# Kernel tuning notes

Measured on AMD Instinct MI355X. Metric: run time of the kernel, lower is better.

The kernel has to match this reference:

```python
import jax, jax.numpy as jnp
import numpy as np

H = 16          # n_heads
DH = 128        # head_dim
DR = 64         # rope_dim
DC = DH - DR    # content_dim = 64
THETA = 10000.0
SCALE = 1.0 / np.sqrt(DH)


def _rope_tables(T, dtype):
    inv = 1.0 / (THETA ** (jnp.arange(0, DR, 2, dtype=jnp.float32) / DR))  # [DR/2]
    t = jnp.arange(T, dtype=jnp.float32)
    freqs = jnp.outer(t, inv)  # [T, DR/2]
    return jnp.cos(freqs).astype(dtype), jnp.sin(freqs).astype(dtype)


def _apply_rope(x, cos, sin):
    # x: [B,H,T,DR]; cos/sin: [T,DR/2] broadcast over B,H
    d = x.shape[-1] // 2
    x1, x2 = x[..., :d], x[..., d:]
    return jnp.concatenate([x1 * cos - x2 * sin, x1 * sin + x2 * cos], axis=-1)


def setup_inputs() -> dict:
    key = jax.random.key(0)
    ks = jax.random.split(key, 9)
    B, T, D = 1, 2048, 2048
    s = 0.02
    return {
        "x": jax.random.normal(ks[0], (B, T, D), jnp.float32),
        "Wq_down": jax.random.normal(ks[1], (D, 512), jnp.float32) * s,
        "Wq_up": jax.random.normal(ks[2], (512, H * DC), jnp.float32) * s,
        "Wq_rope": jax.random.normal(ks[3], (D, H * DR), jnp.float32) * s,
        "Wkv_down": jax.random.normal(ks[4], (D, 512), jnp.float32) * s,
        "Wk_up": jax.random.normal(ks[5], (512, H * DC), jnp.float32) * s,
        "Wv_up": jax.random.normal(ks[6], (512, H * DH), jnp.float32) * s,
        "Wk_rope": jax.random.normal(ks[7], (D, H * DR), jnp.float32) * s,
        "Wo": jax.random.normal(ks[8], (H * DH, D), jnp.float32) * s,
    }


def reference(x, Wq_down, Wq_up, Wq_rope, Wkv_down, Wk_up, Wv_up, Wk_rope, Wo):
    B, T, D = x.shape
    # low-rank query path: down then up, content part only
    q_content = ((x @ Wq_down) @ Wq_up).reshape(B, T, H, DC).transpose(0, 2, 1, 3)
    q_pos = (x @ Wq_rope).reshape(B, T, H, DR).transpose(0, 2, 1, 3)
    kv_latent = x @ Wkv_down                    # [B,T,d_latent]
    k_pos = (x @ Wk_rope).reshape(B, T, H, DR).transpose(0, 2, 1, 3)

    cos, sin = _rope_tables(T, x.dtype)
    q_pos = _apply_rope(q_pos, cos, sin)
    k_pos = _apply_rope(k_pos, cos, sin)

    k_content = (kv_latent @ Wk_up).reshape(B, T, H, DC).transpose(0, 2, 1, 3)
    v = (kv_latent @ Wv_up).reshape(B, T, H, DH).transpose(0, 2, 1, 3)

    q = jnp.concatenate([q_content, q_pos], axis=-1)  # [B,H,T,DH]
    k = jnp.concatenate([k_content, k_pos], axis=-1)  # [B,H,T,DH]

    scores = jnp.einsum("bhtd,bhsd->bhts", q, k) * SCALE
    causal = jnp.tril(jnp.ones((T, T), dtype=bool))
    scores = jnp.where(causal, scores, jnp.finfo(scores.dtype).min)
    attn = jax.nn.softmax(scores, axis=-1)
    out = jnp.einsum("bhts,bhsd->bhtd", attn, v)       # [B,H,T,DH]
    out = out.transpose(0, 2, 1, 3).reshape(B, T, H * DH)
    return out @ Wo
```

## Files before the change

### kernel.cpp

```cpp
#include <hip/hip_runtime.h>
#include <math.h>

#define T_SEQ 2048
#define D_MODEL 2048
#define H_HEADS 16
#define DH 128
#define DR 64
#define DC 64
#define D_LAT 512
#define SEGLEN 14
#define NSEG_TOT 46
#define QSCALE (0.08838834764831845f * 1.4426950408889634f)

typedef __attribute__((ext_vector_type(8))) short short8;
typedef __attribute__((ext_vector_type(4))) short short4v;
typedef __attribute__((ext_vector_type(4))) float f32x4;

#if __has_builtin(__builtin_amdgcn_exp2f)
#define EXP2(x) __builtin_amdgcn_exp2f(x)
#else
#define EXP2(x) exp2f(x)
#endif

__device__ __forceinline__ float bf2f(short b) {
    unsigned u = ((unsigned)(unsigned short)b) << 16;
    return __builtin_bit_cast(float, u);
}
__device__ __forceinline__ short f2bf(float f) {
    unsigned u = __builtin_bit_cast(unsigned, f);
    unsigned r = u + 0x7fffu + ((u >> 16) & 1u);
    return (short)(r >> 16);
}
__device__ __forceinline__ short f2bf_trunc(float f) {
    return (short)(__builtin_bit_cast(unsigned, f) >> 16);
}

#define GLD_LDS(gp, lp) \
    __builtin_amdgcn_global_load_lds( \
        (const __attribute__((address_space(1))) void*)(gp), \
        (__attribute__((address_space(3))) void*)(lp), 16, 0, 0)

__device__ __forceinline__ void ct_tile(float (*tile)[33],
                                        const float* __restrict__ W,
                                        short* __restrict__ Wt,
                                        int R, int C, int ldo, int rel) {
    int bx = rel % (C / 32), by = rel / (C / 32);
    int c0 = bx * 32, r0 = by * 32;
    int tx = threadIdx.x & 31, ty = threadIdx.x >> 5;
    #pragma unroll
    for (int i = 0; i < 4; ++i)
        tile[ty + i * 8][tx] = W[(size_t)(r0 + ty + i * 8) * C + c0 + tx];
    __syncthreads();
    #pragma unroll
    for (int i = 0; i < 4; ++i)
        Wt[(size_t)(c0 + ty + i * 8) * ldo + r0 + tx] = f2bf(tile[tx][ty + i * 8]);
    __syncthreads();
}

__global__ __launch_bounds__(256) void prep(const float* __restrict__ x,
                                            short* __restrict__ xb,
                                            const float* __restrict__ Wqd,
                                            const float* __restrict__ Wkvd,
                                            const float* __restrict__ Wqr,
                                            const float* __restrict__ Wkr,
                                            const float* __restrict__ Wqu,
                                            const float* __restrict__ Wku,
                                            const float* __restrict__ Wvu,
                                            const float* __restrict__ Wo,
                                            short* __restrict__ WdT,
                                            short* __restrict__ WupT2,
                                            short* __restrict__ WoT) {
    __shared__ float tile[32][33];
    int bid = blockIdx.x;
    if (bid < 4096) {
        int i = bid * 1024 + threadIdx.x * 4;
        float4 f = *(const float4*)&x[i];
        short4v o;
        o.x = f2bf(f.x); o.y = f2bf(f.y); o.z = f2bf(f.z); o.w = f2bf(f.w);
        *(short4v*)&xb[i] = o;
    } else if (bid < 5120) {
        ct_tile(tile, Wqd,  WdT + (size_t)0 * 2048,    2048, 512,  2048, bid - 4096);
    } else if (bid < 6144) {
        ct_tile(tile, Wkvd, WdT + (size_t)512 * 2048,  2048, 512,  2048, bid - 5120);
    } else if (bid < 8192) {
        ct_tile(tile, Wqr,  WdT + (size_t)1024 * 2048, 2048, 1024, 2048, bid - 6144);
    } else if (bid < 10240) {
        ct_tile(tile, Wkr,  WdT + (size_t)2048 * 2048, 2048, 1024, 2048, bid - 8192);
    } else if (bid < 10752) {
        ct_tile(tile, Wqu,  WupT2 + (size_t)0 * 512,    512, 1024, 512, bid - 10240);
    } else if (bid < 11264) {
        ct_tile(tile, Wku,  WupT2 + (size_t)1024 * 512, 512, 1024, 512, bid - 10752);
    } else if (bid < 12288) {
        ct_tile(tile, Wvu,  WupT2 + (size_t)2048 * 512, 512, 2048, 512, bid - 11264);
    } else {
        ct_tile(tile, Wo,   WoT, 2048, 2048, 2048, bid - 12288);
    }
}

__global__ __launch_bounds__(256) void transpose_bf16(const short* __restrict__ in,
                                                      short* __restrict__ outb,
                                                      int ldi) {
    __shared__ short tile[64][65];
    int c0 = blockIdx.x * 64, t0 = blockIdx.y * 64;
    int tx = threadIdx.x & 31, ty = threadIdx.x >> 5;
    #pragma unroll
    for (int i = 0; i < 8; ++i) {
        int r = ty + i * 8;
        int vv = *(const int*)&in[(size_t)(t0 + r) * ldi + c0 + tx * 2];
        tile[r][tx * 2]     = (short)(vv & 0xffff);
        tile[r][tx * 2 + 1] = (short)(((unsigned)vv) >> 16);
    }
    __syncthreads();
    #pragma unroll
    for (int i = 0; i < 8; ++i) {
        int c = ty + i * 8;
        unsigned lo = (unsigned short)tile[tx * 2][c];
        unsigned hi = (unsigned short)tile[tx * 2 + 1][c];
        *(int*)&outb[(size_t)(c0 + c) * 2048 + t0 + tx * 2] = (int)(lo | (hi << 16));
    }
}

__global__ __launch_bounds__(256) void gemm_bt(const short* __restrict__ A,
                                               const short* __restrict__ A2,
                                               const short* __restrict__ Bt,
                                               short* __restrict__ C0,
                                               short* __restrict__ C1,
                                               short* __restrict__ C2,
                                               short* __restrict__ C3,
                                               int N, int Kblk,
                                               int lda, int ldb, int ldc,
                                               int ncut, int scut, float cscale) {
    __shared__ short As[128 * 32];
    __shared__ short Bs[128 * 32];
    const int tid = threadIdx.x;
    const int wave = tid >> 6, lane = tid & 63;
    const int lin = blockIdx.x;
    const int X = N >> 7, Xq = X >> 2;
    const int xcd = lin & 7;
    int r = lin >> 3;
    const int bx = (xcd & 3) * Xq + (r % Xq); r /= Xq;
    const int by = (xcd >> 2) * 8 + (r & 7);
    const int bz = r >> 3;
    const int row0 = by * 128, col0 = bx * 128;
    const int kbase = bz * Kblk;
    const short* Ause = (col0 < ncut) ? A : A2;
    short* Cuse = (bz == 0) ? C0 : (bz == 1) ? C1 : (bz == 2) ? C2 : C3;
    const int wr = (wave >> 1) * 64, wc = (wave & 1) * 64;
    const int lr = lane & 15, quad = lane >> 4;

    f32x4 acc[4][4];
    #pragma unroll
    for (int i = 0; i < 4; ++i)
        #pragma unroll
        for (int j = 0; j < 4; ++j) acc[i][j] = (f32x4){0.f, 0.f, 0.f, 0.f};

    for (int k0 = kbase; k0 < kbase + Kblk; k0 += 32) {
        __syncthreads();
        #pragma unroll
        for (int it = 0; it < 2; ++it) {
            int idx = wave * 64 + it * 256 + lane;
            const short* ga = Ause + (size_t)(row0 + (idx >> 2)) * lda + k0 + (idx & 3) * 8;
            const short* gb = Bt   + (size_t)(col0 + (idx >> 2)) * ldb + k0 + (idx & 3) * 8;
            int lds0 = (wave * 64 + it * 256) * 8;
            GLD_LDS(ga, &As[lds0]);
            GLD_LDS(gb, &Bs[lds0]);
        }
        __syncthreads();

        short8 af[4], bfr[4];
        #pragma unroll
        for (int i = 0; i < 4; ++i)
            af[i] = *(const short8*)&As[(wr + i * 16 + lr) * 32 + quad * 8];
        #pragma unroll
        for (int j = 0; j < 4; ++j)
            bfr[j] = *(const short8*)&Bs[(wc + j * 16 + lr) * 32 + quad * 8];
        #pragma unroll
        for (int i = 0; i < 4; ++i)
            #pragma unroll
            for (int j = 0; j < 4; ++j)
                acc[i][j] = __builtin_amdgcn_mfma_f32_16x16x32_bf16(af[i], bfr[j],
                                                                   acc[i][j], 0, 0, 0);
    }

    const float sc = (col0 < scut) ? cscale : 1.0f;
    #pragma unroll
    for (int i = 0; i < 4; ++i) {
        int rb = row0 + wr + i * 16 + quad * 4;
        #pragma unroll
        for (int j = 0; j < 4; ++j) {
            int c = col0 + wc + j * 16 + lr;
            #pragma unroll
            for (int rr = 0; rr < 4; ++rr)
                Cuse[(size_t)(rb + rr) * ldc + c] = f2bf(acc[i][j][rr] * sc);
        }
    }
}

__global__ __launch_bounds__(192) void finish_down(short* __restrict__ cat,
                                                   const short* __restrict__ pdown) {
    const int t = blockIdx.x;
    const int k8 = threadIdx.x * 8;
    const int c0 = ((k8 >> 5) << 6) + (k8 & 31);
    const size_t lo = (size_t)t * 3072 + c0;
    const size_t hi = lo + 32;
    short8 al = *(const short8*)&cat[lo];
    short8 ah = *(const short8*)&cat[hi];
    short8 bl = *(const short8*)&pdown[lo];
    short8 bh = *(const short8*)&pdown[hi];
    float xl[8], xh[8];
    #pragma unroll
    for (int j = 0; j < 8; ++j) {
        xl[j] = bf2f(al[j]) + bf2f(bl[j]);
        xh[j] = bf2f(ah[j]) + bf2f(bh[j]);
    }
    if (c0 >= 1024) {
        float sc = (c0 < 2048) ? QSCALE : 1.0f;
        #pragma unroll
        for (int j = 0; j < 8; ++j) {
            int i = (c0 & 31) + j;
            float freq = (float)t * __powf(10000.0f, -(float)i / 32.0f);
            float cs = __cosf(freq), sn = __sinf(freq);
            float r1 = (xl[j] * cs - xh[j] * sn) * sc;
            float r2 = (xl[j] * sn + xh[j] * cs) * sc;
            xl[j] = r1; xh[j] = r2;
        }
    }
    short8 ol, oh;
    #pragma unroll
    for (int j = 0; j < 8; ++j) { ol[j] = f2bf(xl[j]); oh[j] = f2bf(xh[j]); }
    *(short8*)&cat[lo] = ol;
    *(short8*)&cat[hi] = oh;
}

__global__ __launch_bounds__(256) void add_out_f32(const short* __restrict__ p0,
                                                   const short* __restrict__ p1,
                                                   float* __restrict__ out) {
    int i = (blockIdx.x * 256 + threadIdx.x) * 4;
    short4v a = *(const short4v*)&p0[i];
    short4v b = *(const short4v*)&p1[i];
    float4 o;
    o.x = bf2f(a.x) + bf2f(b.x);
    o.y = bf2f(a.y) + bf2f(b.y);
    o.z = bf2f(a.z) + bf2f(b.z);
    o.w = bf2f(a.w) + bf2f(b.w);
    *(float4*)&out[i] = o;
}

__global__ __launch_bounds__(256) void attn_mla_split(const short* __restrict__ qkup,
                                                      const short* __restrict__ cat,
                                                      const short* __restrict__ vT,
                                                      short* __restrict__ slabA,
                                                      short* __restrict__ slabB,
                                                      float* __restrict__ lpart) {
    const int lin = blockIdx.x;
    const int xcd = lin & 7;
    int k_ = lin >> 3;
    const int h = xcd + 8 * (k_ & 1);
    const int pp = k_ >> 1;
    int qt = 0, s = 0, acc = 0;
    #pragma unroll
    for (int q = 0; q < 16; ++q) {
        const int ns = (4 * q + 4 + SEGLEN - 1) / SEGLEN;
        if (pp >= acc) { qt = q; s = pp - acc; }
        acc += ns;
    }
    const int nchunk = 4 * qt + 4;
    const int nsq = (nchunk + SEGLEN - 1) / SEGLEN;
    const int cbase = nchunk / nsq, crem = nchunk % nsq;
    const int c0 = s * cbase + (s < crem ? s : crem);
    const int c1 = c0 + cbase + (s < crem ? 1 : 0);

    const int tid = threadIdx.x;
    const int wave = tid >> 6, lane = tid & 63;
    const int lr = lane & 15, quad = lane >> 4;

    __shared__ short Ks[2][32 * 128];
    __shared__ short Vst[2][128 * 32];
    __shared__ short Ps[4][2][16 * 40];

    const short8 ones = {0x3F80, 0x3F80, 0x3F80, 0x3F80,
                         0x3F80, 0x3F80, 0x3F80, 0x3F80};

    const int Q0 = qt * 128;
    const int qrowA = Q0 + wave * 16;
    const int qrowB = qrowA + 64;

    short8 qf[2][4];
    #pragma unroll
    for (int sb = 0; sb < 2; ++sb) {
        int t = (sb ? qrowB : qrowA) + lr;
        #pragma unroll
        for (int kci = 0; kci < 4; ++kci) {
            const short* src = (kci < 2)
                ? qkup + (size_t)t * 4096 + h * 64
                : cat + (size_t)t * 3072 + 1024 + h * 64;
            qf[sb][kci] = *(const short8*)&src[(kci & 1) * 32 + quad * 8];
        }
    }

    const int idx = wave * 64 + lane;
    const int key = idx >> 4;
    const int cg = (idx & 15) ^ (key & 15);
    const short* kp0 = (cg < 8)
        ? qkup + (size_t)key * 4096 + 1024 + h * 64 + cg * 8
        : cat + (size_t)key * 3072 + 2048 + h * 64 + (cg - 8) * 8;
    const int kst = (cg < 8) ? 4096 : 3072;
    const short* kp1 = kp0 + (size_t)16 * kst;
    const int dd = idx >> 2;
    const int scg = (idx & 3) ^ (dd & 3);
    const short* vp0 = vT + (size_t)(h * 128 + dd) * 2048 + scg * 8;
    const short* vp1 = vp0 + (size_t)64 * 2048;
    kp0 += (size_t)c0 * 32 * kst; kp1 += (size_t)c0 * 32 * kst;
    vp0 += c0 * 32;               vp1 += c0 * 32;
    const int kadv = 32 * kst;
    const int vadv = 32;
    const int ldsA = (wave * 64) * 8;
    const int ldsB = (wave * 64 + 256) * 8;

    f32x4 Oacc[2][8];
    #pragma unroll
    for (int sb = 0; sb < 2; ++sb)
        #pragma unroll
        for (int d = 0; d < 8; ++d) Oacc[sb][d] = (f32x4){0.f, 0.f, 0.f, 0.f};
    f32x4 Lacc[2];
    Lacc[0] = (f32x4){0.f, 0.f, 0.f, 0.f};
    Lacc[1] = (f32x4){0.f, 0.f, 0.f, 0.f};

    GLD_LDS(kp0, &Ks[0][ldsA]);
    GLD_LDS(kp1, &Ks[0][ldsB]);
    GLD_LDS(vp0, &Vst[0][ldsA]);
    GLD_LDS(vp1, &Vst[0][ldsB]);
    kp0 += kadv; kp1 += kadv; vp0 += vadv; vp1 += vadv;

    int cur = 0;
    for (int c = c0; c < c1; ++c) {
        const int s0 = c * 32;
        const bool havenext = (c + 1 < c1);
        if (havenext) {
            GLD_LDS(kp0, &Ks[cur ^ 1][ldsA]);
            GLD_LDS(kp1, &Ks[cur ^ 1][ldsB]);
            GLD_LDS(vp0, &Vst[cur ^ 1][ldsA]);
            GLD_LDS(vp1, &Vst[cur ^ 1][ldsB]);
            kp0 += kadv; kp1 += kadv; vp0 += vadv; vp1 += vadv;
            asm volatile("s_waitcnt vmcnt(4)" ::: "memory");
        } else {
            asm volatile("s_waitcnt vmcnt(0)" ::: "memory");
        }
        __builtin_amdgcn_s_barrier();

        if (s0 <= qrowB + 15) {
            const bool actA = (s0 <= qrowA + 15);
            const short* Kc = Ks[cur];
            const short* Vc = Vst[cur];

            f32x4 sacc[2][2];
            #pragma unroll
            for (int sb = 0; sb < 2; ++sb)
                #pragma unroll
                for (int n = 0; n < 2; ++n) sacc[sb][n] = (f32x4){0.f, 0.f, 0.f, 0.f};
            #pragma unroll
            for (int n = 0; n < 2; ++n) {
                #pragma unroll
                for (int kci = 0; kci < 4; ++kci) {
                    short8 kf = *(const short8*)
                        &Kc[(n * 16 + lr) * 128 + ((kci * 4 + quad) ^ lr) * 8];
                    if (actA)
                        sacc[0][n] = __builtin_amdgcn_mfma_f32_16x16x32_bf16(
                            qf[0][kci], kf, sacc[0][n], 0, 0, 0);
                    sacc[1][n] = __builtin_amdgcn_mfma_f32_16x16x32_bf16(
                        qf[1][kci], kf, sacc[1][n], 0, 0, 0);
                }
            }
            #pragma unroll
            for (int sb = 0; sb < 2; ++sb) {
                if (sb == 0 && !actA) continue;
                const int qrow0 = sb ? qrowB : qrowA;
                if (s0 + 31 > qrow0) {
                    #pragma unroll
                    for (int r = 0; r < 4; ++r) {
                        int qg = qrow0 + quad * 4 + r;
                        #pragma unroll
                        for (int n = 0; n < 2; ++n) {
                            int sidx = s0 + n * 16 + lr;
                            sacc[sb][n][r] = (sidx <= qg) ? sacc[sb][n][r] : -1e30f;
                        }
                    }
                }
                #pragma unroll
                for (int r = 0; r < 4; ++r) {
                    Ps[wave][sb][(quad * 4 + r) * 40 + lr] =
                        f2bf_trunc(EXP2(sacc[sb][0][r]));
                    Ps[wave][sb][(quad * 4 + r) * 40 + 16 + lr] =
                        f2bf_trunc(EXP2(sacc[sb][1][r]));
                }
            }
            short8 pfA, pfB;
            if (actA) {
                pfA = *(const short8*)&Ps[wave][0][lr * 40 + quad * 8];
                Lacc[0] = __builtin_amdgcn_mfma_f32_16x16x32_bf16(pfA, ones,
                                                                  Lacc[0], 0, 0, 0);
            }
            pfB = *(const short8*)&Ps[wave][1][lr * 40 + quad * 8];
            Lacc[1] = __builtin_amdgcn_mfma_f32_16x16x32_bf16(pfB, ones,
                                                              Lacc[1], 0, 0, 0);
            #pragma unroll
            for (int dt = 0; dt < 8; ++dt) {
                short8 vf = *(const short8*)
                    &Vc[(dt * 16 + lr) * 32 + (quad ^ (lr & 3)) * 8];
                if (actA)
                    Oacc[0][dt] = __builtin_amdgcn_mfma_f32_16x16x32_bf16(
                        pfA, vf, Oacc[0][dt], 0, 0, 0);
                Oacc[1][dt] = __builtin_amdgcn_mfma_f32_16x16x32_bf16(
                    pfB, vf, Oacc[1][dt], 0, 0, 0);
            }
        }

        __builtin_amdgcn_s_barrier();
        cur ^= 1;
    }

    const int slot = h * NSEG_TOT + pp;
    short* slotp = (slot < 512) ? slabA + (size_t)slot * 16384
                                : slabB + (size_t)(slot - 512) * 16384;
    #pragma unroll
    for (int sb = 0; sb < 2; ++sb) {
        const int rbase = wave * 16 + sb * 64 + quad * 4;
        #pragma unroll
        for (int r = 0; r < 4; ++r) {
            #pragma unroll
            for (int dt = 0; dt < 8; ++dt)
                slotp[(rbase + r) * 128 + dt * 16 + lr] = f2bf(Oacc[sb][dt][r]);
        }
        if (lr == 0) {
            #pragma unroll
            for (int r = 0; r < 4; ++r)
                lpart[(size_t)slot * 128 + rbase + r] = Lacc[sb][r];
        }
    }
}

__global__ __launch_bounds__(256) void attn_combine(const short* __restrict__ slabA,
                                                    const short* __restrict__ slabB,
                                                    const float* __restrict__ lpart,
                                                    short* __restrict__ ao) {
    const int t = blockIdx.x;
    const int qt = t >> 7, rl = t & 127;
    const int h = threadIdx.x >> 4;
    const int di = (threadIdx.x & 15) * 8;
    int pf = 0;
    #pragma unroll
    for (int q = 0; q < 16; ++q)
        if (q < qt) pf += (4 * q + 4 + SEGLEN - 1) / SEGLEN;
    const int ns = (4 * qt + 4 + SEGLEN - 1) / SEGLEN;
    float o[8] = {0.f, 0.f, 0.f, 0.f, 0.f, 0.f, 0.f, 0.f};
    float den = 0.f;
    for (int s = 0; s < ns; ++s) {
        const int slot = h * NSEG_TOT + pf + s;
        const short* sp = (slot < 512) ? slabA + (size_t)slot * 16384
                                       : slabB + (size_t)(slot - 512) * 16384;
        short8 v = *(const short8*)&sp[rl * 128 + di];
        #pragma unroll
        for (int j = 0; j < 8; ++j) o[j] += bf2f(v[j]);
        den += lpart[(size_t)slot * 128 + rl];
    }
    float inv = 1.0f / den;
    short8 ov;
    #pragma unroll
    for (int j = 0; j < 8; ++j) ov[j] = f2bf(o[j] * inv);
    *(short8*)&ao[(size_t)t * 2048 + h * 128 + di] = ov;
}

extern "C" void kernel_launch(void* const* d_in, const int* in_sizes, int n_in,
                              void* d_out, int out_size, void* d_ws, size_t ws_size,
                              hipStream_t stream) {
    const float* x        = (const float*)d_in[0];
    const float* Wq_down  = (const float*)d_in[1];
    const float* Wq_up    = (const float*)d_in[2];
    const float* Wq_rope  = (const float*)d_in[3];
    const float* Wkv_down = (const float*)d_in[4];
    const float* Wk_up    = (const float*)d_in[5];
    const float* Wv_up    = (const float*)d_in[6];
    const float* Wk_rope  = (const float*)d_in[7];
    const float* Wo       = (const float*)d_in[8];
    float* out = (float*)d_out;

    short* p = (short*)d_ws;
    short* xb     = p; p += (size_t)2048 * 2048;
    short* WoT    = p; p += (size_t)2048 * 2048;
    short* cat    = p; p += (size_t)2048 * 3072;
    short* upcat2 = p; p += (size_t)2048 * 4096;
    short* WdT    = p; p += (size_t)3072 * 2048;
    short* WupT2  = p; p += (size_t)4096 * 512;
    short* vT     = p; p += (size_t)2048 * 2048;
    float* lpart  = (float*)p;
    short* pdown   = upcat2;
    short* aob     = cat;
    short* slabA   = WdT;
    short* slabB   = xb;
    short* pw0     = upcat2;
    short* pw1     = upcat2 + (size_t)2048 * 2048;

    prep<<<dim3(16384), 256, 0, stream>>>(x, xb, Wq_down, Wkv_down, Wq_rope,
                                          Wk_rope, Wq_up, Wk_up, Wv_up, Wo,
                                          WdT, WupT2, WoT);

    gemm_bt<<<dim3(24 * 16 * 2), 256, 0, stream>>>(xb, xb, WdT, cat, pdown,
                                                   nullptr, nullptr,
                                                   3072, 1024,
                                                   2048, 2048, 3072, 1 << 30, 0, 1.f);

    finish_down<<<dim3(2048), 192, 0, stream>>>(cat, pdown);

    gemm_bt<<<dim3(32 * 16 * 1), 256, 0, stream>>>(cat, cat + 512, WupT2,
                                                   upcat2, nullptr, nullptr, nullptr,
                                                   4096, 512,
                                                   3072, 512, 4096, 1024, 1024, QSCALE);

    transpose_bf16<<<dim3(32, 32), 256, 0, stream>>>(upcat2 + 2048, vT, 4096);

    attn_mla_split<<<dim3(16 * NSEG_TOT), 256, 0, stream>>>(upcat2, cat, vT,
                                                            slabA, slabB, lpart);
    attn_combine<<<dim3(2048), 256, 0, stream>>>(slabA, slabB, lpart, aob);

    gemm_bt<<<dim3(16 * 16 * 2), 256, 0, stream>>>(aob, aob, WoT, pw0, pw1,
                                                   nullptr, nullptr,
                                                   2048, 1024,
                                                   2048, 2048, 2048, 1 << 30, 0, 1.f);
    add_out_f32<<<dim3(2048 * 2048 / 1024), 256, 0, stream>>>(pw0, pw1, out);
}
```

Baseline: 278.7 us.

## Replace double-buffered K/V pipeline with 64-key single-stage loads per iteration

The split attention kernel now works on 64-key chunks instead of 32. Each iteration loads both 32-key halves of K and V into the two LDS buffers at once, waits on a full barrier, then computes both halves. This removes the prefetch of the next chunk and its vmcnt bookkeeping in favour of a simpler load, sync, compute loop with more loads in flight per stage. The trade-off is that load latency is no longer hidden behind compute, and causal masking only skips work at 32-key granularity inside each 64-key chunk. The SEGLEN change keeps the segment count per head unchanged.

```diff
diff --git a/kernel.cpp b/kernel.cpp
--- a/kernel.cpp
+++ b/kernel.cpp
@@ -8,8 +8,9 @@
 #define DR 64
 #define DC 64
 #define D_LAT 512
-#define SEGLEN 14
+#define SEGLEN 7
 #define NSEG_TOT 46
+#define NSEG_OF(q) ((2 * (q) + 2 + SEGLEN - 1) / SEGLEN)
 #define QSCALE (0.08838834764831845f * 1.4426950408889634f)
 
 typedef __attribute__((ext_vector_type(8))) short short8;
@@ -260,12 +261,12 @@
     int qt = 0, s = 0, acc = 0;
     #pragma unroll
     for (int q = 0; q < 16; ++q) {
-        const int ns = (4 * q + 4 + SEGLEN - 1) / SEGLEN;
+        const int ns = NSEG_OF(q);
         if (pp >= acc) { qt = q; s = pp - acc; }
         acc += ns;
     }
-    const int nchunk = 4 * qt + 4;
-    const int nsq = (nchunk + SEGLEN - 1) / SEGLEN;
+    const int nchunk = 2 * qt + 2;
+    const int nsq = NSEG_OF(qt);
     const int cbase = nchunk / nsq, crem = nchunk % nsq;
     const int c0 = s * cbase + (s < crem ? s : crem);
     const int c1 = c0 + cbase + (s < crem ? 1 : 0);
@@ -310,10 +311,11 @@
     const int scg = (idx & 3) ^ (dd & 3);
     const short* vp0 = vT + (size_t)(h * 128 + dd) * 2048 + scg * 8;
     const short* vp1 = vp0 + (size_t)64 * 2048;
-    kp0 += (size_t)c0 * 32 * kst; kp1 += (size_t)c0 * 32 * kst;
-    vp0 += c0 * 32;               vp1 += c0 * 32;
-    const int kadv = 32 * kst;
-    const int vadv = 32;
+    kp0 += (size_t)c0 * 64 * kst; kp1 += (size_t)c0 * 64 * kst;
+    vp0 += c0 * 64;               vp1 += c0 * 64;
+    const int kadv = 64 * kst;
+    const int vadv = 64;
+    const int kph = 32 * kst;
     const int ldsA = (wave * 64) * 8;
     const int ldsB = (wave * 64 + 256) * 8;
 
@@ -326,32 +328,26 @@
     Lacc[0] = (f32x4){0.f, 0.f, 0.f, 0.f};
     Lacc[1] = (f32x4){0.f, 0.f, 0.f, 0.f};
 
-    GLD_LDS(kp0, &Ks[0][ldsA]);
-    GLD_LDS(kp1, &Ks[0][ldsB]);
-    GLD_LDS(vp0, &Vst[0][ldsA]);
-    GLD_LDS(vp1, &Vst[0][ldsB]);
-    kp0 += kadv; kp1 += kadv; vp0 += vadv; vp1 += vadv;
-
-    int cur = 0;
-    for (int c = c0; c < c1; ++c) {
-        const int s0 = c * 32;
-        const bool havenext = (c + 1 < c1);
-        if (havenext) {
-            GLD_LDS(kp0, &Ks[cur ^ 1][ldsA]);
-            GLD_LDS(kp1, &Ks[cur ^ 1][ldsB]);
-            GLD_LDS(vp0, &Vst[cur ^ 1][ldsA]);
-            GLD_LDS(vp1, &Vst[cur ^ 1][ldsB]);
-            kp0 += kadv; kp1 += kadv; vp0 += vadv; vp1 += vadv;
-            asm volatile("s_waitcnt vmcnt(4)" ::: "memory");
-        } else {
-            asm volatile("s_waitcnt vmcnt(0)" ::: "memory");
-        }
-        __builtin_amdgcn_s_barrier();
-
-        if (s0 <= qrowB + 15) {
+    for (int cc = c0; cc < c1; ++cc) {
+        __syncthreads();
+        GLD_LDS(kp0,       &Ks[0][ldsA]);
+        GLD_LDS(kp1,       &Ks[0][ldsB]);
+        GLD_LDS(kp0 + kph, &Ks[1][ldsA]);
+        GLD_LDS(kp1 + kph, &Ks[1][ldsB]);
+        GLD_LDS(vp0,       &Vst[0][ldsA]);
+        GLD_LDS(vp1,       &Vst[0][ldsB]);
+        GLD_LDS(vp0 + 32,  &Vst[1][ldsA]);
+        GLD_LDS(vp1 + 32,  &Vst[1][ldsB]);
+        kp0 += kadv; kp1 += kadv; vp0 += vadv; vp1 += vadv;
+        __syncthreads();
+
+        #pragma unroll
+        for (int half = 0; half < 2; ++half) {
+            const int s0 = cc * 64 + half * 32;
+            if (s0 > qrowB + 15) continue;
             const bool actA = (s0 <= qrowA + 15);
-            const short* Kc = Ks[cur];
-            const short* Vc = Vst[cur];
+            const short* Kc = Ks[half];
+            const short* Vc = Vst[half];
 
             f32x4 sacc[2][2];
             #pragma unroll
@@ -414,9 +410,6 @@
                     pfB, vf, Oacc[1][dt], 0, 0, 0);
             }
         }
-
-        __builtin_amdgcn_s_barrier();
-        cur ^= 1;
     }
 
     const int slot = h * NSEG_TOT + pp;
@@ -450,8 +443,8 @@
     int pf = 0;
     #pragma unroll
     for (int q = 0; q < 16; ++q)
-        if (q < qt) pf += (4 * q + 4 + SEGLEN - 1) / SEGLEN;
-    const int ns = (4 * qt + 4 + SEGLEN - 1) / SEGLEN;
+        if (q < qt) pf += NSEG_OF(q);
+    const int ns = NSEG_OF(qt);
     float o[8] = {0.f, 0.f, 0.f, 0.f, 0.f, 0.f, 0.f, 0.f};
     float den = 0.f;
     for (int s = 0; s < ns; ++s) {
```

Result: no change. 274.4 us (-1.5%).
